# Performance work log

Hardware: AMD Instinct MI355X
Metric: run time of the kernel (lower is better)

## Reference

```python
import jax, jax.numpy as jnp
import numpy as np

B, N, K, D_IN, D, L = 8, 8192, 6, 3, 256, 5
EPS_LN = 1e-5


def layernorm(x, g, b):
    m = jnp.mean(x, axis=-1, keepdims=True)
    v = jnp.mean((x - m) ** 2, axis=-1, keepdims=True)
    return (x - m) * jax.lax.rsqrt(v + EPS_LN) * g + b


def spmm_mean(v, knn):
    # sparse adj matmul: out[j] = sum_{n: j in knn[n]} v[n], then / k
    n, k = knn.shape[-2], knn.shape[-1]
    src = jnp.repeat(jnp.arange(n), k)  # [N*K]

    def one(vb, kb):
        return jnp.zeros_like(vb).at[kb.reshape(-1)].add(vb[src])

    return jax.vmap(one)(v, knn) / (k + 1e-6)


def grf_layer(h, knn, qkv_w, out_w, out_b, hops=3):
    q, k, v = jnp.split(h @ qkv_w, 3, axis=-1)
    for _ in range(hops):
        v = spmm_mean(v, knn)
        k = spmm_mean(k, knn)
    attn = jnp.sum(q * k, axis=-1, keepdims=True)
    return (attn * v) @ out_w + out_b


def linear_attention(h, qkv_w, out_w, out_b):
    q, k, v = jnp.split(h @ qkv_w, 3, axis=-1)
    q = jax.nn.relu(q) + 1e-6
    k = jax.nn.relu(k) + 1e-6
    kv = jnp.einsum('bnd,bne->bde', k, v)
    z = 1.0 / (jnp.einsum('bnd,bd->bn', q, k.sum(axis=1)) + 1e-6)
    attn = jnp.einsum('bnd,bde,bn->bne', q, kv, z)
    return attn @ out_w + out_b


def setup_inputs() -> dict:
    key = jax.random.key(0)
    ks = jax.random.split(key, 12)
    s = 0.02
    return {
        'x': jax.random.normal(ks[0], (B, N, D_IN), jnp.float32),
        'knn': jax.random.randint(ks[1], (B, N, K), 0, N, jnp.int32),
        'emb_w': jax.random.normal(ks[2], (D_IN, D), jnp.float32) * s,
        'emb_b': jnp.zeros((D,), jnp.float32),
        'norm_g': jnp.ones((2 * L, D), jnp.float32),
        'norm_b': jnp.zeros((2 * L, D), jnp.float32),
        'grf_qkv': jax.random.normal(ks[3], (L, D, 3 * D), jnp.float32) * s,
        'grf_outw': jax.random.normal(ks[4], (L, D, D), jnp.float32) * s,
        'grf_outb': jnp.zeros((L, D), jnp.float32),
        'attn_qkv': jax.random.normal(ks[5], (L, D, 3 * D), jnp.float32) * s,
        'attn_outw': jax.random.normal(ks[6], (L, D, D), jnp.float32) * s,
        'attn_outb': jnp.zeros((L, D), jnp.float32),
        'head_w': jax.random.normal(ks[7], (D, 3), jnp.float32) * s,
        'head_b': jnp.zeros((3,), jnp.float32),
    }


def reference(x, knn, emb_w, emb_b, norm_g, norm_b, grf_qkv, grf_outw, grf_outb,
              attn_qkv, attn_outw, attn_outb, head_w, head_b):
    h = x @ emb_w + emb_b
    for i in range(L):
        h = h + grf_layer(layernorm(h, norm_g[2 * i], norm_b[2 * i]), knn,
                          grf_qkv[i], grf_outw[i], grf_outb[i])
        h = h + linear_attention(layernorm(h, norm_g[2 * i + 1], norm_b[2 * i + 1]),
                                 attn_qkv[i], attn_outw[i], attn_outb[i])
    return h @ head_w + head_b
```

## Files before the change

### kernel.cpp

```cpp
#include <hip/hip_runtime.h>

#define BB 8
#define NN 8192
#define KK 6
#define DD 256
#define LL 5
#define NE (BB*NN*KK)
#define PLANE (NN*DD)
#define INV6 (1.0f/6.000001f)

typedef unsigned short u16;
typedef __attribute__((ext_vector_type(8))) _Float16 h8;
typedef __attribute__((ext_vector_type(8))) unsigned short us8;
typedef __attribute__((ext_vector_type(4))) float f32x4;

__device__ __forceinline__ u16 f2h(float f){
  union { _Float16 h; u16 u; } c; c.h = (_Float16)f; return c.u;
}
__device__ __forceinline__ float h2f(u16 u){
  union { _Float16 h; u16 u; } c; c.u = u; return (float)c.h;
}

__device__ __forceinline__ void ldscp(const u16* g, u16* l){
  __builtin_amdgcn_global_load_lds(
      (const __attribute__((address_space(1))) void*)g,
      (__attribute__((address_space(3))) void*)l, 16, 0, 0);
}

__global__ void k_count(const int* __restrict__ knn, int* __restrict__ off){
  int e = blockIdx.x*256 + threadIdx.x;
  if(e >= NE) return;
  int b = e / (NN*KK);
  int j = knn[e];
  atomicAdd(&off[b*(NN+1) + 1 + j], 1);
}

__global__ __launch_bounds__(1024) void k_scan(int* __restrict__ offAll){
  __shared__ int lds[1024];
  __shared__ int carry_s;
  int* off = offAll + blockIdx.x*(NN+1);
  const int len = NN+1;
  int t = threadIdx.x;
  if(t==0) carry_s = 0;
  __syncthreads();
  for(int base=0; base<len; base+=1024){
    int x = (base+t < len) ? off[base+t] : 0;
    lds[t] = x; __syncthreads();
    for(int s=1; s<1024; s<<=1){
      int v = (t>=s) ? lds[t-s] : 0;
      __syncthreads();
      lds[t] += v;
      __syncthreads();
    }
    int incl = lds[t];
    int carry = carry_s;
    __syncthreads();
    if(base+t < len) off[base+t] = incl + carry;
    if(t==1023) carry_s = carry + incl;
    __syncthreads();
  }
}

__global__ void k_fill(const int* __restrict__ knn, int* __restrict__ cursor, int* __restrict__ srcE){
  int e = blockIdx.x*256 + threadIdx.x;
  if(e >= NE) return;
  int b = e / (NN*KK);
  int n = (e % (NN*KK)) / KK;
  int j = knn[e];
  int pos = atomicAdd(&cursor[b*(NN+1) + j], 1);
  srcE[(long)b*NN*KK + pos] = n;
}

__global__ __launch_bounds__(256) void k_prepw(const float* __restrict__ W, u16* __restrict__ Wt, int N){
  int n = blockIdx.x, l = blockIdx.y, k = threadIdx.x;
  float x = W[((long)l*256 + k)*N + n];
  u16 hb = f2h(x);
  Wt[(((long)l*2 + 0)*N + n)*256 + k] = hb;
  Wt[(((long)l*2 + 1)*N + n)*256 + k] = f2h(x - h2f(hb));
}

__global__ __launch_bounds__(256) void k_embed(const float* __restrict__ x, const float* __restrict__ ew,
                        const float* __restrict__ eb, float* __restrict__ h){
  int g = blockIdx.x, z = blockIdx.y, d = threadIdx.x;
  const float* xp = x + ((long)z*NN + g)*3;
  h[(long)z*PLANE + (long)g*DD + d] = xp[0]*ew[0*DD+d] + xp[1]*ew[1*DD+d] + xp[2]*ew[2*DD+d] + eb[d];
}

__global__ __launch_bounds__(256) void k_ln(const float* __restrict__ h, const float* __restrict__ g,
                     const float* __restrict__ bia, u16* __restrict__ out){
  long z = blockIdx.y;
  int row = blockIdx.x*4 + (threadIdx.x >> 6);
  int lane = threadIdx.x & 63;
  const float4 x = *(const float4*)(h + z*PLANE + (long)row*DD + lane*4);
  float s  = x.x + x.y + x.z + x.w;
  float s2 = x.x*x.x + x.y*x.y + x.z*x.z + x.w*x.w;
  for(int o=1;o<64;o<<=1){ s += __shfl_xor(s,o); s2 += __shfl_xor(s2,o); }
  float m = s*(1.0f/256.0f);
  float var = s2*(1.0f/256.0f) - m*m;
  float r = rsqrtf(var + 1e-5f);
  const float4 gu = *(const float4*)(g + lane*4);
  const float4 bu = *(const float4*)(bia + lane*4);
  ushort4 o4;
  o4.x = f2h((x.x-m)*r*gu.x + bu.x);
  o4.y = f2h((x.y-m)*r*gu.y + bu.y);
  o4.z = f2h((x.z-m)*r*gu.z + bu.z);
  o4.w = f2h((x.w-m)*r*gu.w + bu.w);
  *(ushort4*)(out + z*PLANE + (long)row*DD + lane*4) = o4;
}

template<int BM,int BN,bool ASPLIT,bool BF32,bool BSPLIT>
__global__ __launch_bounds__(256) void k_mgemm(
    const u16* __restrict__ A, long aStride, long aLoOff, int K, int kSplit,
    const void* __restrict__ Bv, long bStride, long bLoOff,
    const float* __restrict__ rowscale, long rsStride,
    const float* __restrict__ bias,
    u16* __restrict__ o0, u16* __restrict__ o1, u16* __restrict__ o2,
    long oStride, int reluMask, long oLoOff,
    float* __restrict__ accOut, long hStride)
{
  constexpr int WM = BM/2, WN = BN/2, MT = WM/16, NT = WN/16;
  constexpr int STG1 = BM*32*(ASPLIT?2:1) + BN*32*(BSPLIT?2:1);
  constexpr int STGT = BF32 ? STG1 : 2*STG1;
  constexpr int EPI = (BM==128) ? 32*132*2 : 0;
  constexpr int SM  = (STGT > EPI) ? STGT : EPI;
  __shared__ __align__(16) u16 smem[SM];
  float* epi = (float*)smem;

  const int t = threadIdx.x;
  const int nz = blockIdx.z;
  const long z = nz / kSplit;
  const int chunk = nz % kSplit;
  const int kLen = K / kSplit, kLo = chunk * kLen;
  const int rowTile = blockIdx.x*BM, colTile = blockIdx.y*BN;
  const int l = t & 63, w = t >> 6;
  const int wr = w >> 1, wc = w & 1;
  const int lm = l & 15, kq = l >> 4;

  f32x4 acc[MT][NT];
  #pragma unroll
  for(int mt=0;mt<MT;mt++)
    #pragma unroll
    for(int nt=0;nt<NT;nt++) acc[mt][nt] = (f32x4){0.f,0.f,0.f,0.f};

  if constexpr (!BF32){
    auto stageAB = [&](int buf, int k0){
      u16* Ahi_ = smem + (size_t)buf*STG1;
      u16* Alo_ = Ahi_ + BM*32;
      u16* Bhi_ = Ahi_ + BM*32*(ASPLIT?2:1);
      u16* Blo_ = Bhi_ + BN*32;
      {
        constexpr int NCH = BM/64;
        #pragma unroll
        for(int li=0; li<NCH; li++){
          int f = li*256 + t;
          int row = f>>2, c = (f&3)*8;
          const u16* gp = A + z*aStride + (long)(rowTile+row)*K + k0 + c;
          ldscp(gp, &Ahi_[f*8]);
          if constexpr (ASPLIT) ldscp(gp + aLoOff, &Alo_[f*8]);
        }
      }
      {
        constexpr int NCH = BN/64;
        #pragma unroll
        for(int li=0; li<NCH; li++){
          int f = li*256 + t;
          int row = f>>2, c = (f&3)*8;
          const u16* gp = (const u16*)Bv + z*bStride + (long)(colTile+row)*K + k0 + c;
          ldscp(gp, &Bhi_[f*8]);
          if constexpr (BSPLIT) ldscp(gp + bLoOff, &Blo_[f*8]);
        }
      }
    };

    const int nsteps = kLen >> 5;
    stageAB(0, kLo);
    __syncthreads();
    int cur = 0;
    for(int ks=0; ks<nsteps; ++ks){
      if(ks+1 < nsteps) stageAB(cur^1, kLo + ((ks+1)<<5));
      const u16* Ahi_ = smem + (size_t)cur*STG1;
      const u16* Alo_ = Ahi_ + BM*32;
      const u16* Bhi_ = Ahi_ + BM*32*(ASPLIT?2:1);
      const u16* Blo_ = Bhi_ + BN*32;
      h8 ah[MT], al[MT], bh[NT], bl[NT];
      #pragma unroll
      for(int mt=0;mt<MT;mt++){
        int idx = (wr*WM + mt*16 + lm)*32 + kq*8;
        ah[mt] = *(const h8*)&Ahi_[idx];
        if constexpr (ASPLIT) al[mt] = *(const h8*)&Alo_[idx];
      }
      #pragma unroll
      for(int nt=0;nt<NT;nt++){
        int idx = (wc*WN + nt*16 + lm)*32 + kq*8;
        bh[nt] = *(const h8*)&Bhi_[idx];
        if constexpr (BSPLIT) bl[nt] = *(const h8*)&Blo_[idx];
      }
      #pragma unroll
      for(int mt=0;mt<MT;mt++)
        #pragma unroll
        for(int nt=0;nt<NT;nt++){
          acc[mt][nt] = __builtin_amdgcn_mfma_f32_16x16x32_f16(ah[mt], bh[nt], acc[mt][nt], 0, 0, 0);
          if constexpr (BSPLIT)
            acc[mt][nt] = __builtin_amdgcn_mfma_f32_16x16x32_f16(ah[mt], bl[nt], acc[mt][nt], 0, 0, 0);
          if constexpr (ASPLIT)
            acc[mt][nt] = __builtin_amdgcn_mfma_f32_16x16x32_f16(al[mt], bh[nt], acc[mt][nt], 0, 0, 0);
        }
      __syncthreads();
      cur ^= 1;
    }
  } else {
    u16* Ahi = smem;
    u16* Alo = smem + BM*32;
    u16* Bhi = smem + BM*32*(ASPLIT?2:1);
    u16* Blo = Bhi + BN*32;
    for(int k0=kLo; k0<kLo+kLen; k0+=32){
      __syncthreads();
      {
        constexpr int NCH = BM/64;
        #pragma unroll
        for(int li=0; li<NCH; li++){
          int f = li*256 + t;
          int row = f>>2, c = (f&3)*8;
          const u16* gp = A + z*aStride + (long)(rowTile+row)*K + k0 + c;
          ldscp(gp, &Ahi[f*8]);
          if constexpr (ASPLIT) ldscp(gp + aLoOff, &Alo[f*8]);
        }
      }
      {
        constexpr int NCH = BN/64;
        #pragma unroll
        for(int li=0; li<NCH; li++){
          int f = li*256 + t;
          int row = f>>2, c = (f&3)*8;
          const float* src = (const float*)Bv + z*bStride + (long)(colTile+row)*K + k0 + c;
          float4 v0 = ((const float4*)src)[0], v1 = ((const float4*)src)[1];
          us8 hv;
          hv[0]=f2h(v0.x); hv[1]=f2h(v0.y); hv[2]=f2h(v0.z); hv[3]=f2h(v0.w);
          hv[4]=f2h(v1.x); hv[5]=f2h(v1.y); hv[6]=f2h(v1.z); hv[7]=f2h(v1.w);
          *(us8*)&Bhi[f*8] = hv;
        }
      }
      __syncthreads();
      h8 ah[MT], al[MT], bh[NT];
      #pragma unroll
      for(int mt=0;mt<MT;mt++){
        int idx = (wr*WM + mt*16 + lm)*32 + kq*8;
        ah[mt] = *(const h8*)&Ahi[idx];
        if constexpr (ASPLIT) al[mt] = *(const h8*)&Alo[idx];
      }
      #pragma unroll
      for(int nt=0;nt<NT;nt++){
        int idx = (wc*WN + nt*16 + lm)*32 + kq*8;
        bh[nt] = *(const h8*)&Bhi[idx];
      }
      #pragma unroll
      for(int mt=0;mt<MT;mt++)
        #pragma unroll
        for(int nt=0;nt<NT;nt++){
          acc[mt][nt] = __builtin_amdgcn_mfma_f32_16x16x32_f16(ah[mt], bh[nt], acc[mt][nt], 0, 0, 0);
          if constexpr (ASPLIT)
            acc[mt][nt] = __builtin_amdgcn_mfma_f32_16x16x32_f16(al[mt], bh[nt], acc[mt][nt], 0, 0, 0);
        }
    }
  }

  if constexpr (BM == 128){
    const int sec = colTile >> 8;
    u16* osec = (sec==0) ? o0 : ((sec==1) ? o1 : o2);
    const bool relu = (reluMask >> sec) & 1;
    #pragma unroll
    for(int mt=0;mt<MT;mt++){
      __syncthreads();
      #pragma unroll
      for(int r=0;r<4;r++){
        int gm = rowTile + wr*64 + mt*16 + kq*4 + r;
        float sc = rowscale ? rowscale[z*rsStride + gm] : 1.0f;
        int rl = wr*16 + kq*4 + r;
        #pragma unroll
        for(int nt=0;nt<NT;nt++)
          epi[rl*132 + wc*64 + nt*16 + lm] = acc[mt][nt][r]*sc;
      }
      __syncthreads();
      #pragma unroll
      for(int ss=0;ss<2;ss++){
        int s = ss*256 + t;
        int rl = s >> 4, sc8 = (s & 15)*8;
        int gm2 = rowTile + (rl>>4)*64 + mt*16 + (rl & 15);
        float v[8];
        #pragma unroll
        for(int j=0;j<8;j++) v[j] = epi[rl*132 + sc8 + j];
        if(bias){
          const float* bp = bias + colTile + sc8;
          #pragma unroll
          for(int j=0;j<8;j++) v[j] += bp[j];
        }
        if(accOut){
          float* hp = accOut + z*hStride + (long)gm2*256 + colTile + sc8;
          float4 h0 = ((float4*)hp)[0], h1 = ((float4*)hp)[1];
          h0.x += v[0]; h0.y += v[1]; h0.z += v[2]; h0.w += v[3];
          h1.x += v[4]; h1.y += v[5]; h1.z += v[6]; h1.w += v[7];
          ((float4*)hp)[0] = h0; ((float4*)hp)[1] = h1;
        } else {
          us8 o8;
          #pragma unroll
          for(int j=0;j<8;j++){
            float vv = v[j];
            if(relu) vv = fmaxf(vv, 0.f) + 1e-6f;
            o8[j] = f2h(vv);
          }
          *(us8*)(osec + z*oStride + (long)gm2*256 + ((colTile + sc8) & 255)) = o8;
        }
      }
    }
  } else {
    #pragma unroll
    for(int mt=0;mt<MT;mt++){
      #pragma unroll
      for(int r=0;r<4;r++){
        int gm = rowTile + wr*WM + mt*16 + kq*4 + r;
        float sc = rowscale ? rowscale[z*rsStride + gm] : 1.0f;
        if(accOut){
          float* hp = accOut + z*hStride + (long)gm*256;
          if(kSplit > 1){
            #pragma unroll
            for(int nt=0;nt<NT;nt++){
              int gc = colTile + wc*WN + nt*16 + lm;
              atomicAdd(&hp[gc], acc[mt][nt][r]);
            }
          } else {
            #pragma unroll
            for(int nt=0;nt<NT;nt++){
              int gc = colTile + wc*WN + nt*16 + lm;
              hp[gc] += acc[mt][nt][r]*sc + (bias ? bias[gc] : 0.f);
            }
          }
        } else {
          #pragma unroll
          for(int nt=0;nt<NT;nt++){
            int gc = colTile + wc*WN + nt*16 + lm;
            int sec = gc >> 8;
            u16* o = (sec==0) ? o0 : ((sec==1) ? o1 : o2);
            float val = acc[mt][nt][r]*sc + (bias ? bias[gc] : 0.f);
            if((reluMask >> sec) & 1) val = fmaxf(val, 0.f) + 1e-6f;
            if(sec==0 && oLoOff){
              u16* oo = o0 + 2*z*oStride + (long)gm*256 + (gc & 255);
              u16 hb = f2h(val);
              oo[0] = hb;
              oo[oLoOff] = f2h(val - h2f(hb));
            } else {
              o[z*oStride + (long)gm*256 + (gc & 255)] = f2h(val);
            }
          }
        }
      }
    }
  }
}

__global__ __launch_bounds__(256) void k_fusedout(
    const u16* __restrict__ A, const u16* __restrict__ B, long bStride, long bLoOff,
    const float* __restrict__ rowscale, const float* __restrict__ bias,
    float* __restrict__ h,
    const float* __restrict__ lnG, const float* __restrict__ lnB,
    u16* __restrict__ Lout)
{
  __shared__ __align__(16) u16 smem[16384];
  u16* Bh = smem;
  u16* Bl = smem + 8192;
  float* epi = (float*)smem;

  const int t = threadIdx.x;
  const long z = blockIdx.z;
  const int rowTile = blockIdx.x*32;
  const int l = t & 63, w = t >> 6;
  const int wr = w >> 1, wc = w & 1;
  const int lm = l & 15, kq = l >> 4;
  const u16* Ab = A + z*PLANE;
  const u16* Bb = B + z*bStride;

  f32x4 acc[8];
  #pragma unroll
  for(int nt=0;nt<8;nt++) acc[nt] = (f32x4){0.f,0.f,0.f,0.f};

  h8 areg[8];
  {
    const u16* arow = Ab + (long)(rowTile + wr*16 + lm)*256 + kq*8;
    #pragma unroll
    for(int kk=0;kk<8;kk++) areg[kk] = *(const h8*)(arow + kk*32);
  }

  #pragma unroll
  for(int kk=0; kk<8; ++kk){
    __syncthreads();
    #pragma unroll
    for(int li=0; li<4; li++){
      int f = li*256 + t;
      int row = f>>2, c = (f&3)*8;
      const u16* gp = Bb + (long)row*256 + kk*32 + c;
      ldscp(gp, &Bh[f*8]);
      ldscp(gp + bLoOff, &Bl[f*8]);
    }
    __syncthreads();
    #pragma unroll
    for(int nt=0;nt<8;nt++){
      int idx = (wc*128 + nt*16 + lm)*32 + kq*8;
      const h8 bhf = *(const h8*)&Bh[idx];
      const h8 blf = *(const h8*)&Bl[idx];
      acc[nt] = __builtin_amdgcn_mfma_f32_16x16x32_f16(areg[kk], bhf, acc[nt], 0, 0, 0);
      acc[nt] = __builtin_amdgcn_mfma_f32_16x16x32_f16(areg[kk], blf, acc[nt], 0, 0, 0);
    }
  }

  #pragma unroll
  for(int p=0;p<2;p++){
    __syncthreads();
    if(wr == p){
      #pragma unroll
      for(int r=0;r<4;r++){
        int rl = kq*4 + r;
        int gm = rowTile + p*16 + rl;
        float sc = rowscale ? rowscale[z*NN + gm] : 1.0f;
        #pragma unroll
        for(int nt=0;nt<8;nt++)
          epi[rl*260 + wc*128 + nt*16 + lm] = acc[nt][r]*sc;
      }
    }
    __syncthreads();
    #pragma unroll
    for(int ss=0;ss<4;ss++){
      int s = ss*256 + t;
      int rl = s >> 6;
      int c4 = (s & 63)*4;
      int gm = rowTile + p*16 + rl;
      float4 e = *(float4*)&epi[rl*260 + c4];
      float4 x;
      x.x = e.x + bias[c4+0];
      x.y = e.y + bias[c4+1];
      x.z = e.z + bias[c4+2];
      x.w = e.w + bias[c4+3];
      float* hp = h + z*PLANE + (long)gm*256 + c4;
      float4 h0 = *(float4*)hp;
      x.x += h0.x; x.y += h0.y; x.z += h0.z; x.w += h0.w;
      *(float4*)hp = x;
      if(lnG){
        float sA = x.x + x.y + x.z + x.w;
        float s2 = x.x*x.x + x.y*x.y + x.z*x.z + x.w*x.w;
        for(int o=1;o<64;o<<=1){ sA += __shfl_xor(sA,o); s2 += __shfl_xor(s2,o); }
        float m = sA*(1.0f/256.0f);
        float var = s2*(1.0f/256.0f) - m*m;
        float rr = rsqrtf(var + 1e-5f);
        const float4 gu = *(const float4*)(lnG + c4);
        const float4 bu = *(const float4*)(lnB + c4);
        ushort4 o4;
        o4.x = f2h((x.x-m)*rr*gu.x + bu.x);
        o4.y = f2h((x.y-m)*rr*gu.y + bu.y);
        o4.z = f2h((x.z-m)*rr*gu.z + bu.z);
        o4.w = f2h((x.w-m)*rr*gu.w + bu.w);
        *(ushort4*)(Lout + z*PLANE + (long)gm*256 + c4) = o4;
      }
    }
  }
}

template<int MODE>
__global__ __launch_bounds__(256) void k_spmm2(
    const u16* __restrict__ kin, const u16* __restrict__ vin,
    const int* __restrict__ offB, const int* __restrict__ srcB,
    u16* __restrict__ kout, u16* __restrict__ vout,
    const u16* __restrict__ q, float* __restrict__ rs){
  long z = blockIdx.x;
  const int* off = offB + z*(NN+1);
  const int* sE  = srcB + z*(long)NN*KK;

  if constexpr (MODE == 0){
    const u16* kp = kin + z*PLANE;
    const u16* vp = vin + z*PLANE;
    int row = blockIdx.y*16 + (threadIdx.x >> 4);
    int d8 = blockIdx.z*128 + (threadIdx.x & 15)*8;
    int s0 = off[row], s1 = off[row+1];
    float ak[8], av[8];
    #pragma unroll
    for(int j=0;j<8;j++){ ak[j]=0.f; av[j]=0.f; }
    int e = s0;
    for(; e+1 < s1; e += 2){
      int n0 = sE[e], n1 = sE[e+1];
      us8 k0 = *(const us8*)(kp + (long)n0*DD + d8);
      us8 k1 = *(const us8*)(kp + (long)n1*DD + d8);
      us8 v0 = *(const us8*)(vp + (long)n0*DD + d8);
      us8 v1 = *(const us8*)(vp + (long)n1*DD + d8);
      #pragma unroll
      for(int j=0;j<8;j++){
        ak[j] += h2f(k0[j]) + h2f(k1[j]);
        av[j] += h2f(v0[j]) + h2f(v1[j]);
      }
    }
    if(e < s1){
      int n0 = sE[e];
      us8 k0 = *(const us8*)(kp + (long)n0*DD + d8);
      us8 v0 = *(const us8*)(vp + (long)n0*DD + d8);
      #pragma unroll
      for(int j=0;j<8;j++){ ak[j] += h2f(k0[j]); av[j] += h2f(v0[j]); }
    }
    us8 ok, ov;
    #pragma unroll
    for(int j=0;j<8;j++){ ok[j] = f2h(ak[j]*INV6); ov[j] = f2h(av[j]*INV6); }
    *(us8*)(kout + z*PLANE + (long)row*DD + d8) = ok;
    *(us8*)(vout + z*PLANE + (long)row*DD + d8) = ov;
  } else {
    if(blockIdx.z == 0){
      const u16* kp = kin + z*PLANE;
      int row = blockIdx.y*8 + (threadIdx.x >> 5);
      int l32 = threadIdx.x & 31;
      int d8 = l32*8;
      int s0 = off[row], s1 = off[row+1];
      float ak[8];
      #pragma unroll
      for(int j=0;j<8;j++) ak[j]=0.f;
      int e = s0;
      for(; e+1 < s1; e += 2){
        int n0 = sE[e], n1 = sE[e+1];
        us8 k0 = *(const us8*)(kp + (long)n0*DD + d8);
        us8 k1 = *(const us8*)(kp + (long)n1*DD + d8);
        #pragma unroll
        for(int j=0;j<8;j++) ak[j] += h2f(k0[j]) + h2f(k1[j]);
      }
      if(e < s1){
        int n0 = sE[e];
        us8 k0 = *(const us8*)(kp + (long)n0*DD + d8);
        #pragma unroll
        for(int j=0;j<8;j++) ak[j] += h2f(k0[j]);
      }
      us8 qv = *(const us8*)(q + z*PLANE + (long)row*DD + d8);
      float s = 0.f;
      #pragma unroll
      for(int j=0;j<8;j++) s += h2f(qv[j]) * ak[j];
      for(int o=1;o<32;o<<=1) s += __shfl_xor(s,o);
      if(l32==0) rs[z*NN + row] = s*INV6;
    } else {
      const u16* vp = vin + z*PLANE;
      int row = (blockIdx.y & 511)*16 + (threadIdx.x >> 4);
      int d8 = (blockIdx.y >> 9)*128 + (threadIdx.x & 15)*8;
      int s0 = off[row], s1 = off[row+1];
      float av[8];
      #pragma unroll
      for(int j=0;j<8;j++) av[j]=0.f;
      int e = s0;
      for(; e+1 < s1; e += 2){
        int n0 = sE[e], n1 = sE[e+1];
        us8 v0 = *(const us8*)(vp + (long)n0*DD + d8);
        us8 v1 = *(const us8*)(vp + (long)n1*DD + d8);
        #pragma unroll
        for(int j=0;j<8;j++) av[j] += h2f(v0[j]) + h2f(v1[j]);
      }
      if(e < s1){
        int n0 = sE[e];
        us8 v0 = *(const us8*)(vp + (long)n0*DD + d8);
        #pragma unroll
        for(int j=0;j<8;j++) av[j] += h2f(v0[j]);
      }
      us8 ov;
      #pragma unroll
      for(int j=0;j<8;j++) ov[j] = f2h(av[j]*INV6);
      *(us8*)(vout + z*PLANE + (long)row*DD + d8) = ov;
    }
  }
}

__global__ __launch_bounds__(256) void k_zcalc(const u16* __restrict__ q, const float* __restrict__ ksum,
                        float* __restrict__ rs){
  long z = blockIdx.y;
  int row = blockIdx.x*4 + (threadIdx.x >> 6);
  int lane = threadIdx.x & 63;
  ushort4 qv = *(const ushort4*)(q + z*PLANE + (long)row*DD + lane*4);
  const float4 c = *(const float4*)(ksum + z*DD + lane*4);
  float s = h2f(qv.x)*c.x + h2f(qv.y)*c.y + h2f(qv.z)*c.z + h2f(qv.w)*c.w;
  for(int o=1;o<64;o<<=1) s += __shfl_xor(s,o);
  if(lane==0) rs[z*NN + row] = 1.0f / (s + 1e-6f);
}

__global__ __launch_bounds__(256) void k_transp2(
    const u16* __restrict__ in0, u16* __restrict__ out0,
    const u16* __restrict__ in1, u16* __restrict__ out1){
  __shared__ u16 tile[64][72];
  int zz = blockIdx.z;
  long z = zz >> 1;
  const u16* ip = ((zz & 1) ? in1 : in0) + z*PLANE;
  u16* op = ((zz & 1) ? out1 : out0) + z*PLANE;
  int r0 = blockIdx.x*64, c0 = blockIdx.y*64;
  int t = threadIdx.x;
  {
    int r = t>>2, cg = (t&3)*16;
    *(us8*)&tile[r][cg]   = *(const us8*)(ip + (long)(r0+r)*DD + c0 + cg);
    *(us8*)&tile[r][cg+8] = *(const us8*)(ip + (long)(r0+r)*DD + c0 + cg + 8);
  }
  __syncthreads();
  {
    int c = t>>2, rg = t&3;
    us8 a, b;
    #pragma unroll
    for(int j=0;j<8;j++){ a[j] = tile[rg*16+j][c]; b[j] = tile[rg*16+8+j][c]; }
    u16* dst = op + (long)(c0+c)*NN + r0 + rg*16;
    *(us8*)dst = a; *(us8*)(dst+8) = b;
  }
}

__global__ __launch_bounds__(256) void k_ksum(const u16* __restrict__ kT, float* __restrict__ ksum){
  long z = blockIdx.y;
  int d = blockIdx.x;
  const u16* p = kT + z*PLANE + (long)d*NN;
  float s = 0.f;
  for(int i=threadIdx.x*8; i<NN; i+=2048){
    us8 a = *(const us8*)(p+i);
    #pragma unroll
    for(int j=0;j<8;j++) s += h2f(a[j]);
  }
  for(int o=1;o<64;o<<=1) s += __shfl_xor(s,o);
  __shared__ float ws4[4];
  int w = threadIdx.x >> 6;
  if((threadIdx.x & 63)==0) ws4[w] = s;
  __syncthreads();
  if(threadIdx.x==0) ksum[z*DD + d] = ws4[0]+ws4[1]+ws4[2]+ws4[3];
}

__global__ __launch_bounds__(256) void k_head(const float* __restrict__ h, const float* __restrict__ hw,
                       const float* __restrict__ hb, float* __restrict__ out){
  long z = blockIdx.y;
  int row = blockIdx.x*4 + (threadIdx.x >> 6);
  int lane = threadIdx.x & 63;
  const float4 x = *(const float4*)(h + z*PLANE + (long)row*DD + lane*4);
  int d0 = lane*4;
  float a0 = x.x*hw[(d0+0)*3+0] + x.y*hw[(d0+1)*3+0] + x.z*hw[(d0+2)*3+0] + x.w*hw[(d0+3)*3+0];
  float a1 = x.x*hw[(d0+0)*3+1] + x.y*hw[(d0+1)*3+1] + x.z*hw[(d0+2)*3+1] + x.w*hw[(d0+3)*3+1];
  float a2 = x.x*hw[(d0+0)*3+2] + x.y*hw[(d0+1)*3+2] + x.z*hw[(d0+2)*3+2] + x.w*hw[(d0+3)*3+2];
  for(int o=1;o<64;o<<=1){
    a0 += __shfl_xor(a0,o); a1 += __shfl_xor(a1,o); a2 += __shfl_xor(a2,o);
  }
  if(lane==0){
    float* op = out + (z*NN + row)*3;
    op[0] = a0 + hb[0];
    op[1] = a1 + hb[1];
    op[2] = a2 + hb[2];
  }
}

struct Carve {
  float *h; u16 *L,*Q,*Bp,*Cp,*T;
  float *kvf; u16 *w2t;
  float *ksum,*rs;
  int *off,*cursor,*srcE;
  u16 *wt_gqkv,*wt_aqkv,*wt_gout,*wt_aout;
  size_t total;
};

static Carve carve(char* base, int C){
  Carve c;
  size_t cur = 0;
  auto bump = [&](size_t bytes)->char*{
    char* p = base ? base + cur : (char*)0;
    cur += (bytes + 255) & ~(size_t)255;
    return p;
  };
  c.h    = (float*)bump((size_t)C*PLANE*4);
  c.L    = (u16*)bump((size_t)C*PLANE*2);
  c.Q    = (u16*)bump((size_t)C*PLANE*2);
  c.Bp   = (u16*)bump((size_t)C*PLANE*2);
  c.Cp   = (u16*)bump((size_t)C*PLANE*2);
  c.T    = (u16*)bump((size_t)C*PLANE*2);
  c.kvf  = (float*)bump((size_t)C*DD*DD*4);
  c.w2t  = (u16*)bump((size_t)C*2*DD*DD*2);
  c.ksum = (float*)bump((size_t)C*DD*4);
  c.rs   = (float*)bump((size_t)C*NN*4);
  c.off  = (int*)bump((size_t)BB*(NN+1)*4);
  c.cursor=(int*)bump((size_t)BB*(NN+1)*4);
  c.srcE = (int*)bump((size_t)NE*4);
  c.wt_gqkv = (u16*)bump((size_t)LL*2*768*256*2);
  c.wt_aqkv = (u16*)bump((size_t)LL*2*768*256*2);
  c.wt_gout = (u16*)bump((size_t)LL*2*256*256*2);
  c.wt_aout = (u16*)bump((size_t)LL*2*256*256*2);
  c.total = cur;
  return c;
}

extern "C" void kernel_launch(void* const* d_in, const int* in_sizes, int n_in,
                              void* d_out, int out_size, void* d_ws, size_t ws_size,
                              hipStream_t stream)
{
  const float* x        = (const float*)d_in[0];
  const int*   knn      = (const int*)d_in[1];
  const float* emb_w    = (const float*)d_in[2];
  const float* emb_b    = (const float*)d_in[3];
  const float* norm_g   = (const float*)d_in[4];
  const float* norm_b   = (const float*)d_in[5];
  const float* grf_qkv  = (const float*)d_in[6];
  const float* grf_outw = (const float*)d_in[7];
  const float* grf_outb = (const float*)d_in[8];
  const float* attn_qkv = (const float*)d_in[9];
  const float* attn_outw= (const float*)d_in[10];
  const float* attn_outb= (const float*)d_in[11];
  const float* head_w   = (const float*)d_in[12];
  const float* head_b   = (const float*)d_in[13];
  float* out = (float*)d_out;

  int C = 1;
  for(int cc=BB; cc>=1; cc>>=1){ if(carve(nullptr, cc).total <= ws_size){ C = cc; break; } }
  Carve ws = carve((char*)d_ws, C);

  k_prepw<<<dim3(768, LL), 256, 0, stream>>>(grf_qkv,  ws.wt_gqkv, 768);
  k_prepw<<<dim3(768, LL), 256, 0, stream>>>(attn_qkv, ws.wt_aqkv, 768);
  k_prepw<<<dim3(256, LL), 256, 0, stream>>>(grf_outw, ws.wt_gout, 256);
  k_prepw<<<dim3(256, LL), 256, 0, stream>>>(attn_outw,ws.wt_aout, 256);

  hipMemsetAsync(ws.off, 0, (size_t)BB*(NN+1)*sizeof(int), stream);
  k_count<<<dim3((NE+255)/256), 256, 0, stream>>>(knn, ws.off);
  k_scan<<<dim3(BB), 1024, 0, stream>>>(ws.off);
  hipMemcpyAsync(ws.cursor, ws.off, (size_t)BB*(NN+1)*sizeof(int), hipMemcpyDeviceToDevice, stream);
  k_fill<<<dim3((NE+255)/256), 256, 0, stream>>>(knn, ws.cursor, ws.srcE);

  const long PL = PLANE;
  for(int b0=0; b0<BB; b0+=C){
    const int* offB  = ws.off  + (long)b0*(NN+1);
    const int* srcB  = ws.srcE + (long)b0*NN*KK;

    k_embed<<<dim3(NN, C), 256, 0, stream>>>(x + (long)b0*NN*3, emb_w, emb_b, ws.h);
    k_ln<<<dim3(NN/4, C), 256, 0, stream>>>(ws.h, norm_g, norm_b, ws.L);

    for(int i=0; i<LL; i++){
      k_mgemm<128,128,false,false,true><<<dim3(64, 6, C), 256, 0, stream>>>(
          ws.L, PL, 0, 256, 1,
          ws.wt_gqkv + (long)i*2*768*256, 0, (long)768*256,
          nullptr, 0, nullptr,
          ws.Q, ws.Bp, ws.Cp, PL, 0, 0, nullptr, 0);
      k_spmm2<0><<<dim3(C, NN/16, 2), 256, 0, stream>>>(ws.Bp, ws.Cp, offB, srcB, ws.L, ws.T, nullptr, nullptr);
      k_spmm2<0><<<dim3(C, NN/16, 2), 256, 0, stream>>>(ws.L,  ws.T,  offB, srcB, ws.Bp, ws.Cp, nullptr, nullptr);
      k_spmm2<1><<<dim3(C, NN/8, 2), 256, 0, stream>>>(ws.Bp, ws.Cp, offB, srcB, nullptr, ws.T, ws.Q, ws.rs);
      k_fusedout<<<dim3(NN/32, 1, C), 256, 0, stream>>>(
          ws.T, ws.wt_gout + (long)i*2*256*256, 0, (long)256*256,
          ws.rs, grf_outb + (long)i*DD, ws.h,
          norm_g + (2*i+1)*DD, norm_b + (2*i+1)*DD, ws.L);

      k_mgemm<128,128,false,false,true><<<dim3(64, 6, C), 256, 0, stream>>>(
          ws.L, PL, 0, 256, 1,
          ws.wt_aqkv + (long)i*2*768*256, 0, (long)768*256,
          nullptr, 0, nullptr,
          ws.Q, ws.Bp, ws.Cp, PL, 3 , 0, nullptr, 0);
      k_transp2<<<dim3(NN/64, DD/64, 2*C), 256, 0, stream>>>(ws.Bp, ws.L, ws.Cp, ws.T);
      k_ksum<<<dim3(DD, C), 256, 0, stream>>>(ws.L, ws.ksum);
      hipMemsetAsync(ws.kvf, 0, (size_t)C*DD*DD*sizeof(float), stream);
      k_mgemm<64,64,false,false,false><<<dim3(4, 4, C*8), 256, 0, stream>>>(
          ws.L, PL, 0, NN, 8,
          ws.T, PL, 0,
          nullptr, 0, nullptr,
          nullptr, nullptr, nullptr, 0, 0, 0, ws.kvf, (long)DD*DD);
      k_mgemm<64,64,true,true,false><<<dim3(4, 4, C), 256, 0, stream>>>(
          ws.wt_aout + (long)i*2*256*256, 0, (long)256*256, 256, 1,
          ws.kvf, (long)DD*DD, 0,
          nullptr, 0, nullptr,
          ws.w2t, nullptr, nullptr, (long)DD*DD, 0, (long)DD*DD,
          nullptr, 0);
      k_zcalc<<<dim3(NN/4, C), 256, 0, stream>>>(ws.Q, ws.ksum, ws.rs);
      const float* g2 = (i==LL-1) ? nullptr : norm_g + (2*i+2)*DD;
      const float* b2 = (i==LL-1) ? nullptr : norm_b + (2*i+2)*DD;
      k_fusedout<<<dim3(NN/32, 1, C), 256, 0, stream>>>(
          ws.Q, ws.w2t, 2L*DD*DD, (long)DD*DD,
          ws.rs, attn_outb + (long)i*DD, ws.h,
          g2, b2, ws.L);
    }

    k_head<<<dim3(NN/4, C), 256, 0, stream>>>(ws.h, head_w, head_b, out + (long)b0*NN*3);
  }
}
```

Before: 2.555 ms.

## Fuse ksum into transpose, z-normalizer into output GEMM, and head into final layer

Removes three small kernels. The key column sum is now accumulated with atomics inside the transpose kernel, after a memset. The linear-attention normalizer is computed from the A registers already loaded in the fused output kernel. The head projection is folded into the last fused-output epilogue. This cuts launches and extra passes over Q and the transposed K, at the cost of atomic contention on ksum and extra register use in the fused kernel.

```diff
diff --git a/kernel.cpp b/kernel.cpp
--- a/kernel.cpp
+++ b/kernel.cpp
@@ -212,7 +212,6 @@
     u16* Ahi = smem;
     u16* Alo = smem + BM*32;
     u16* Bhi = smem + BM*32*(ASPLIT?2:1);
-    u16* Blo = Bhi + BN*32;
     for(int k0=kLo; k0<kLo+kLen; k0+=32){
       __syncthreads();
       {
@@ -359,10 +358,13 @@
 
 __global__ __launch_bounds__(256) void k_fusedout(
     const u16* __restrict__ A, const u16* __restrict__ B, long bStride, long bLoOff,
-    const float* __restrict__ rowscale, const float* __restrict__ bias,
+    const float* __restrict__ rowscale, const float* __restrict__ ksumIn,
+    const float* __restrict__ bias,
     float* __restrict__ h,
     const float* __restrict__ lnG, const float* __restrict__ lnB,
-    u16* __restrict__ Lout)
+    u16* __restrict__ Lout,
+    const float* __restrict__ headW, const float* __restrict__ headB,
+    float* __restrict__ headOut)
 {
   __shared__ __align__(16) u16 smem[16384];
   u16* Bh = smem;
@@ -389,6 +391,24 @@
     for(int kk=0;kk<8;kk++) areg[kk] = *(const h8*)(arow + kk*32);
   }
 
+  float rsv = 0.f;
+  if(ksumIn){
+    const float* kb = ksumIn + z*DD;
+    float s = 0.f;
+    #pragma unroll
+    for(int kk=0;kk<8;kk++){
+      const float4 c0v = *(const float4*)(kb + kq*8 + kk*32);
+      const float4 c1v = *(const float4*)(kb + kq*8 + kk*32 + 4);
+      s += (float)areg[kk][0]*c0v.x + (float)areg[kk][1]*c0v.y
+         + (float)areg[kk][2]*c0v.z + (float)areg[kk][3]*c0v.w
+         + (float)areg[kk][4]*c1v.x + (float)areg[kk][5]*c1v.y
+         + (float)areg[kk][6]*c1v.z + (float)areg[kk][7]*c1v.w;
+    }
+    s += __shfl_xor(s, 16);
+    s += __shfl_xor(s, 32);
+    rsv = 1.0f/(s + 1e-6f);
+  }
+
   #pragma unroll
   for(int kk=0; kk<8; ++kk){
     __syncthreads();
@@ -419,7 +439,9 @@
       for(int r=0;r<4;r++){
         int rl = kq*4 + r;
         int gm = rowTile + p*16 + rl;
-        float sc = rowscale ? rowscale[z*NN + gm] : 1.0f;
+        float sc;
+        if(ksumIn) sc = __shfl(rsv, kq*4 + r);
+        else       sc = rowscale ? rowscale[z*NN + gm] : 1.0f;
         #pragma unroll
         for(int nt=0;nt<8;nt++)
           epi[rl*260 + wc*128 + nt*16 + lm] = acc[nt][r]*sc;
@@ -457,6 +479,20 @@
         o4.z = f2h((x.z-m)*rr*gu.z + bu.z);
         o4.w = f2h((x.w-m)*rr*gu.w + bu.w);
         *(ushort4*)(Lout + z*PLANE + (long)gm*256 + c4) = o4;
+      } else if(headW){
+        int d0 = c4;
+        float a0 = x.x*headW[(d0+0)*3+0] + x.y*headW[(d0+1)*3+0] + x.z*headW[(d0+2)*3+0] + x.w*headW[(d0+3)*3+0];
+        float a1 = x.x*headW[(d0+0)*3+1] + x.y*headW[(d0+1)*3+1] + x.z*headW[(d0+2)*3+1] + x.w*headW[(d0+3)*3+1];
+        float a2 = x.x*headW[(d0+0)*3+2] + x.y*headW[(d0+1)*3+2] + x.z*headW[(d0+2)*3+2] + x.w*headW[(d0+3)*3+2];
+        for(int o=1;o<64;o<<=1){
+          a0 += __shfl_xor(a0,o); a1 += __shfl_xor(a1,o); a2 += __shfl_xor(a2,o);
+        }
+        if((t & 63)==0){
+          float* op = headOut + ((long)z*NN + gm)*3;
+          op[0] = a0 + headB[0];
+          op[1] = a1 + headB[1];
+          op[2] = a2 + headB[2];
+        }
       }
     }
   }
@@ -566,21 +602,10 @@
   }
 }
 
-__global__ __launch_bounds__(256) void k_zcalc(const u16* __restrict__ q, const float* __restrict__ ksum,
-                        float* __restrict__ rs){
-  long z = blockIdx.y;
-  int row = blockIdx.x*4 + (threadIdx.x >> 6);
-  int lane = threadIdx.x & 63;
-  ushort4 qv = *(const ushort4*)(q + z*PLANE + (long)row*DD + lane*4);
-  const float4 c = *(const float4*)(ksum + z*DD + lane*4);
-  float s = h2f(qv.x)*c.x + h2f(qv.y)*c.y + h2f(qv.z)*c.z + h2f(qv.w)*c.w;
-  for(int o=1;o<64;o<<=1) s += __shfl_xor(s,o);
-  if(lane==0) rs[z*NN + row] = 1.0f / (s + 1e-6f);
-}
-
 __global__ __launch_bounds__(256) void k_transp2(
     const u16* __restrict__ in0, u16* __restrict__ out0,
-    const u16* __restrict__ in1, u16* __restrict__ out1){
+    const u16* __restrict__ in1, u16* __restrict__ out1,
+    float* __restrict__ ksum){
   __shared__ u16 tile[64][72];
   int zz = blockIdx.z;
   long z = zz >> 1;
@@ -601,45 +626,14 @@
     for(int j=0;j<8;j++){ a[j] = tile[rg*16+j][c]; b[j] = tile[rg*16+8+j][c]; }
     u16* dst = op + (long)(c0+c)*NN + r0 + rg*16;
     *(us8*)dst = a; *(us8*)(dst+8) = b;
-  }
-}
-
-__global__ __launch_bounds__(256) void k_ksum(const u16* __restrict__ kT, float* __restrict__ ksum){
-  long z = blockIdx.y;
-  int d = blockIdx.x;
-  const u16* p = kT + z*PLANE + (long)d*NN;
-  float s = 0.f;
-  for(int i=threadIdx.x*8; i<NN; i+=2048){
-    us8 a = *(const us8*)(p+i);
-    #pragma unroll
-    for(int j=0;j<8;j++) s += h2f(a[j]);
-  }
-  for(int o=1;o<64;o<<=1) s += __shfl_xor(s,o);
-  __shared__ float ws4[4];
-  int w = threadIdx.x >> 6;
-  if((threadIdx.x & 63)==0) ws4[w] = s;
-  __syncthreads();
-  if(threadIdx.x==0) ksum[z*DD + d] = ws4[0]+ws4[1]+ws4[2]+ws4[3];
-}
-
-__global__ __launch_bounds__(256) void k_head(const float* __restrict__ h, const float* __restrict__ hw,
-                       const float* __restrict__ hb, float* __restrict__ out){
-  long z = blockIdx.y;
-  int row = blockIdx.x*4 + (threadIdx.x >> 6);
-  int lane = threadIdx.x & 63;
-  const float4 x = *(const float4*)(h + z*PLANE + (long)row*DD + lane*4);
-  int d0 = lane*4;
-  float a0 = x.x*hw[(d0+0)*3+0] + x.y*hw[(d0+1)*3+0] + x.z*hw[(d0+2)*3+0] + x.w*hw[(d0+3)*3+0];
-  float a1 = x.x*hw[(d0+0)*3+1] + x.y*hw[(d0+1)*3+1] + x.z*hw[(d0+2)*3+1] + x.w*hw[(d0+3)*3+1];
-  float a2 = x.x*hw[(d0+0)*3+2] + x.y*hw[(d0+1)*3+2] + x.z*hw[(d0+2)*3+2] + x.w*hw[(d0+3)*3+2];
-  for(int o=1;o<64;o<<=1){
-    a0 += __shfl_xor(a0,o); a1 += __shfl_xor(a1,o); a2 += __shfl_xor(a2,o);
-  }
-  if(lane==0){
-    float* op = out + (z*NN + row)*3;
-    op[0] = a0 + hb[0];
-    op[1] = a1 + hb[1];
-    op[2] = a2 + hb[2];
+    if((zz & 1)==0){
+      float p = 0.f;
+      #pragma unroll
+      for(int j=0;j<8;j++) p += h2f(a[j]) + h2f(b[j]);
+      p += __shfl_xor(p, 1);
+      p += __shfl_xor(p, 2);
+      if(rg == 0) atomicAdd(&ksum[z*DD + c0 + c], p);
+    }
   }
 }
 
@@ -735,16 +729,17 @@
       k_spmm2<1><<<dim3(C, NN/8, 2), 256, 0, stream>>>(ws.Bp, ws.Cp, offB, srcB, nullptr, ws.T, ws.Q, ws.rs);
       k_fusedout<<<dim3(NN/32, 1, C), 256, 0, stream>>>(
           ws.T, ws.wt_gout + (long)i*2*256*256, 0, (long)256*256,
-          ws.rs, grf_outb + (long)i*DD, ws.h,
-          norm_g + (2*i+1)*DD, norm_b + (2*i+1)*DD, ws.L);
+          ws.rs, nullptr, grf_outb + (long)i*DD, ws.h,
+          norm_g + (2*i+1)*DD, norm_b + (2*i+1)*DD, ws.L,
+          nullptr, nullptr, nullptr);
 
       k_mgemm<128,128,false,false,true><<<dim3(64, 6, C), 256, 0, stream>>>(
           ws.L, PL, 0, 256, 1,
           ws.wt_aqkv + (long)i*2*768*256, 0, (long)768*256,
           nullptr, 0, nullptr,
           ws.Q, ws.Bp, ws.Cp, PL, 3 , 0, nullptr, 0);
-      k_transp2<<<dim3(NN/64, DD/64, 2*C), 256, 0, stream>>>(ws.Bp, ws.L, ws.Cp, ws.T);
-      k_ksum<<<dim3(DD, C), 256, 0, stream>>>(ws.L, ws.ksum);
+      hipMemsetAsync(ws.ksum, 0, (size_t)C*DD*sizeof(float), stream);
+      k_transp2<<<dim3(NN/64, DD/64, 2*C), 256, 0, stream>>>(ws.Bp, ws.L, ws.Cp, ws.T, ws.ksum);
       hipMemsetAsync(ws.kvf, 0, (size_t)C*DD*DD*sizeof(float), stream);
       k_mgemm<64,64,false,false,false><<<dim3(4, 4, C*8), 256, 0, stream>>>(
           ws.L, PL, 0, NN, 8,
@@ -757,15 +752,15 @@
           nullptr, 0, nullptr,
           ws.w2t, nullptr, nullptr, (long)DD*DD, 0, (long)DD*DD,
           nullptr, 0);
-      k_zcalc<<<dim3(NN/4, C), 256, 0, stream>>>(ws.Q, ws.ksum, ws.rs);
       const float* g2 = (i==LL-1) ? nullptr : norm_g + (2*i+2)*DD;
       const float* b2 = (i==LL-1) ? nullptr : norm_b + (2*i+2)*DD;
       k_fusedout<<<dim3(NN/32, 1, C), 256, 0, stream>>>(
           ws.Q, ws.w2t, 2L*DD*DD, (long)DD*DD,
-          ws.rs, attn_outb + (long)i*DD, ws.h,
-          g2, b2, ws.L);
-    }
-
-    k_head<<<dim3(NN/4, C), 256, 0, stream>>>(ws.h, head_w, head_b, out + (long)b0*NN*3);
-  }
-}
+          nullptr, ws.ksum, attn_outb + (long)i*DD, ws.h,
+          g2, b2, ws.L,
+          (i==LL-1) ? head_w : nullptr,
+          (i==LL-1) ? head_b : nullptr,
+          (i==LL-1) ? (out + (long)b0*NN*3) : nullptr);
+    }
+  }
+}
```

Result: faster. 2.466 ms, median of 2 (-3.5%).
